# Kernel optimization log

Measured on AMD Instinct MI355X. Metric: run time of the kernel, lower is better.

The kernel has to match this reference:

```python
import jax, jax.numpy as jnp
import numpy as np

SESSION_CHANNELS = [128, 160, 192, 224, 240, 248, 252, 256]  # per-session channel counts
N_SESS = len(SESSION_CHANNELS)
B, MAX_C, MAX_T = 16, 256, 4096
HID, N_SRC = 512, 256


def setup_inputs() -> dict:
    key = jax.random.key(0)
    ks = jax.random.split(key, 7)
    session_ids = jax.random.randint(ks[0], (B,), 0, N_SESS)
    chan_table = jnp.asarray(SESSION_CHANNELS)
    channel_counts = chan_table[session_ids]
    seq_lens = jax.random.randint(ks[1], (B,), MAX_T // 2, MAX_T + 1)
    x = jax.random.normal(ks[2], (B, MAX_C, MAX_T), jnp.float32)
    # zero-pad beyond true channels and true time (as the docstring states)
    cmask = (jnp.arange(MAX_C)[None, :] < channel_counts[:, None]).astype(x.dtype)
    tmask = (jnp.arange(MAX_T)[None, :] < seq_lens[:, None]).astype(x.dtype)
    x = x * cmask[:, :, None] * tmask[:, None, :]
    # per-session Linear(num_channels -> HID), padded to MAX_C rows (torch-style uniform init)
    lim1 = 1.0 / np.sqrt(MAX_C)
    W_sess = jax.random.uniform(ks[3], (N_SESS, MAX_C, HID), jnp.float32, -lim1, lim1)
    b_sess = jax.random.uniform(ks[4], (N_SESS, HID), jnp.float32, -lim1, lim1)
    lim2 = 1.0 / np.sqrt(HID)
    W2 = jax.random.uniform(ks[5], (HID, N_SRC), jnp.float32, -lim2, lim2)
    b2 = jax.random.uniform(ks[6], (N_SRC,), jnp.float32, -lim2, lim2)
    return dict(x=x, session_ids=session_ids, channel_counts=channel_counts,
                seq_lens=seq_lens, W_sess=W_sess, b_sess=b_sess, W2=W2, b2=b2)


def reference(x, session_ids, channel_counts, seq_lens, W_sess, b_sess, W2, b2):
    # mask padded channels so the full-width contraction equals the sliced per-sample matmul
    cmask = (jnp.arange(x.shape[1])[None, :] < channel_counts[:, None]).astype(x.dtype)
    xm = x * cmask[:, :, None]                       # (B, Max_C, Max_T)
    W = W_sess[session_ids]                          # (B, Max_C, HID) gathered per sample
    b = b_sess[session_ids]                          # (B, HID)
    h = jnp.einsum('bct,bch->bht', xm, W) + b[:, :, None]
    h = jax.nn.gelu(h, approximate=False)            # torch nn.GELU default is exact erf
    out = jnp.einsum('bht,hs->bst', h, W2) + b2[None, :, None]  # (B, N_SRC, Max_T)
    tmask = (jnp.arange(x.shape[2])[None, :] < seq_lens[:, None]).astype(x.dtype)
    return out * tmask[:, None, :]
```

## Files before the change

### kernel.cpp

```cpp
#include <hip/hip_runtime.h>

typedef __attribute__((ext_vector_type(8))) _Float16 f16x8;
typedef __attribute__((ext_vector_type(4))) _Float16 f16x4;
typedef __attribute__((ext_vector_type(2))) __fp16 fp16v2;
typedef __attribute__((ext_vector_type(4))) float f32x4;

#define NB 16
#define MAXC 256
#define MAXT 4096
#define HID 512
#define NSRC 256

#define BAR() asm volatile("s_waitcnt lgkmcnt(0)\n\ts_barrier" ::: "memory")

#define MFMA(a, b, c) __builtin_amdgcn_mfma_f32_16x16x32_f16(a, b, c, 0, 0, 0)

__device__ __forceinline__ float gelu_fast(float x) {
  float p = x * x;
  float q = __builtin_fmaf(p, -0.10294336f, -2.30220778f);
  float e = __builtin_amdgcn_exp2f(x * q);
  return x * __builtin_amdgcn_rcpf(1.0f + e);
}

__global__ void transpose_cvt_kernel(const float* __restrict__ src,
                                     _Float16* __restrict__ dst, int R, int C) {
  __shared__ float tile[32][33];
  const float* s = src + (size_t)blockIdx.z * R * C;
  _Float16* d = dst + (size_t)blockIdx.z * R * C;
  int c0 = blockIdx.x * 32, r0 = blockIdx.y * 32;
  int tx = threadIdx.x, ty = threadIdx.y;
  for (int i = ty; i < 32; i += 8)
    tile[i][tx] = s[(size_t)(r0 + i) * C + (c0 + tx)];
  __syncthreads();
  for (int i = ty; i < 32; i += 8)
    d[(size_t)(c0 + i) * R + (r0 + tx)] = (_Float16)tile[tx][i];
}

__global__ __launch_bounds__(256)
void transpose_x_kernel(const float* __restrict__ x,
                        const int* __restrict__ seq_lens,
                        _Float16* __restrict__ xT) {
  int b = blockIdx.z;
  int seqlen = seq_lens[b];
  int t0 = blockIdx.x * 64;
  if (t0 >= ((seqlen + 127) & ~127)) return;
  int c0 = blockIdx.y * 64;
  __shared__ float tile[64][65];
  int tid = threadIdx.x;
  int tx = tid & 63, ty = tid >> 6;
  const float* xp = x + ((size_t)b * MAXC + c0) * MAXT + t0;
  #pragma unroll
  for (int i = 0; i < 16; ++i) {
    int c = ty + i * 4;
    tile[c][tx] = xp[(size_t)c * MAXT + tx];
  }
  __syncthreads();
  int wt = tid >> 5;
  int c2 = (tid & 31) * 2;
  _Float16* op = xT + ((size_t)b * MAXT + t0) * MAXC + c0;
  #pragma unroll
  for (int i = 0; i < 8; ++i) {
    int tl = wt + i * 8;
    fp16v2 p = __builtin_amdgcn_cvt_pkrtz(tile[c2][tl], tile[c2 + 1][tl]);
    *(fp16v2*)(op + (size_t)tl * MAXC + c2) = p;
  }
}


__global__ __launch_bounds__(256, 4)
void gemm1_kernel(const _Float16* __restrict__ xT,
                  const int* __restrict__ sess_ids,
                  const int* __restrict__ seq_lens,
                  const _Float16* __restrict__ W1t,
                  const float* __restrict__ b_sess,
                  _Float16* __restrict__ h_t) {
  int wg = blockIdx.x;
  int nt = wg & 31;
  int mt = (wg >> 5) & 3;
  int b = wg >> 7;
  int tb0 = nt * 128, h0 = mt * 128;
  int seqlen = seq_lens[b];
  if (tb0 >= seqlen) return;
  int sid = sess_ids[b];

  __shared__ _Float16 As[128 * 64];
  __shared__ _Float16 Bs[128 * 64];

  int tid = threadIdx.x;
  int lane = tid & 63, w = tid >> 6;
  int wr = w >> 1, wc = w & 1;
  int lg = lane >> 4, lr = lane & 15;

  f32x4 acc[4][4];
  #pragma unroll
  for (int mi = 0; mi < 4; ++mi) {
    f32x4 bv = *(const f32x4*)(b_sess + sid * HID + h0 + wr * 64 + mi * 16 + lg * 4);
    #pragma unroll
    for (int ni = 0; ni < 4; ++ni) acc[mi][ni] = bv;
  }

  int ar = tid >> 1, ah = tid & 1;
  const _Float16* WA = W1t + (size_t)sid * HID * MAXC + (size_t)(h0 + ar) * MAXC + ah * 32;
  const _Float16* HB = xT + ((size_t)b * MAXT + tb0 + ar) * MAXC + ah * 32;

  #pragma unroll 1
  for (int kc = 0; kc < 4; ++kc) {
    int k0 = kc * 64;
    #pragma unroll
    for (int j = 0; j < 4; ++j) {
      f16x8 v = *(const f16x8*)(WA + k0 + j * 8);
      *(f16x8*)(&As[ar * 64 + (((ah * 4 + j) ^ (ar & 7)) * 8)]) = v;
    }
    #pragma unroll
    for (int j = 0; j < 4; ++j) {
      f16x8 v = *(const f16x8*)(HB + k0 + j * 8);
      *(f16x8*)(&Bs[ar * 64 + (((ah * 4 + j) ^ (ar & 7)) * 8)]) = v;
    }
    BAR();
    #pragma unroll
    for (int slot = 0; slot < 2; ++slot) {
      f16x8 af[4], bf[4];
      #pragma unroll
      for (int mi = 0; mi < 4; ++mi) {
        int row = wr * 64 + mi * 16 + lr;
        af[mi] = *(const f16x8*)(&As[row * 64 + (((slot * 4 + lg) ^ (row & 7)) * 8)]);
      }
      #pragma unroll
      for (int ni = 0; ni < 4; ++ni) {
        int t = wc * 64 + ni * 16 + lr;
        bf[ni] = *(const f16x8*)(&Bs[t * 64 + (((slot * 4 + lg) ^ (t & 7)) * 8)]);
      }
      __builtin_amdgcn_s_setprio(1);
      #pragma unroll
      for (int mi = 0; mi < 4; ++mi)
        #pragma unroll
        for (int ni = 0; ni < 4; ++ni)
          acc[mi][ni] = MFMA(af[mi], bf[ni], acc[mi][ni]);
      __builtin_amdgcn_s_setprio(0);
    }
    BAR();
  }

  _Float16* hp = h_t + (size_t)b * MAXT * HID;
  #pragma unroll
  for (int mi = 0; mi < 4; ++mi) {
    int h = h0 + wr * 64 + mi * 16 + lg * 4;
    #pragma unroll
    for (int ni = 0; ni < 4; ++ni) {
      int t = tb0 + wc * 64 + ni * 16 + lr;
      f16x4 g;
      #pragma unroll
      for (int r = 0; r < 4; ++r) g[r] = (_Float16)gelu_fast(acc[mi][ni][r]);
      *(f16x4*)(hp + (size_t)t * HID + h) = g;
    }
  }
}

__global__ __launch_bounds__(256, 4)
void gemm2_kernel(const int* __restrict__ seq_lens,
                  const _Float16* __restrict__ W2t,
                  const float* __restrict__ b2,
                  const _Float16* __restrict__ h_t,
                  float* __restrict__ out) {
  int wg = blockIdx.x;
  int nt = wg & 31;
  int mt = (wg >> 5) & 1;
  int b = wg >> 6;
  int tb0 = nt * 128, s0 = mt * 128;
  int seqlen = seq_lens[b];
  int tid = threadIdx.x;

  if (tb0 >= seqlen) {
    int sr = tid >> 1, tq = (tid & 1) * 64;
    float* po = out + ((size_t)b * NSRC + s0 + sr) * MAXT + tb0 + tq;
    f32x4 z = {0.f, 0.f, 0.f, 0.f};
    #pragma unroll
    for (int i = 0; i < 16; ++i) *(f32x4*)(po + i * 4) = z;
    return;
  }

  __shared__ _Float16 As[128 * 64];
  __shared__ _Float16 Bs[128 * 64];

  int lane = tid & 63, w = tid >> 6;
  int wr = w >> 1, wc = w & 1;
  int lg = lane >> 4, lr = lane & 15;

  f32x4 acc[4][4];
  #pragma unroll
  for (int mi = 0; mi < 4; ++mi) {
    f32x4 bv = *(const f32x4*)(b2 + s0 + wr * 64 + mi * 16 + lg * 4);
    #pragma unroll
    for (int ni = 0; ni < 4; ++ni) acc[mi][ni] = bv;
  }

  int ar = tid >> 1, ah = tid & 1;
  const _Float16* WA = W2t + (size_t)(s0 + ar) * HID + ah * 32;
  const _Float16* HB = h_t + ((size_t)b * MAXT + tb0 + ar) * HID + ah * 32;

  #pragma unroll 1
  for (int kc = 0; kc < 8; ++kc) {
    int k0 = kc * 64;
    #pragma unroll
    for (int j = 0; j < 4; ++j) {
      f16x8 v = *(const f16x8*)(WA + k0 + j * 8);
      *(f16x8*)(&As[ar * 64 + (((ah * 4 + j) ^ (ar & 7)) * 8)]) = v;
    }
    #pragma unroll
    for (int j = 0; j < 4; ++j) {
      f16x8 v = *(const f16x8*)(HB + k0 + j * 8);
      *(f16x8*)(&Bs[ar * 64 + (((ah * 4 + j) ^ (ar & 7)) * 8)]) = v;
    }
    BAR();
    #pragma unroll
    for (int slot = 0; slot < 2; ++slot) {
      f16x8 af[4], bf[4];
      #pragma unroll
      for (int mi = 0; mi < 4; ++mi) {
        int row = wr * 64 + mi * 16 + lr;
        af[mi] = *(const f16x8*)(&As[row * 64 + (((slot * 4 + lg) ^ (row & 7)) * 8)]);
      }
      #pragma unroll
      for (int ni = 0; ni < 4; ++ni) {
        int t = wc * 64 + ni * 16 + lr;
        bf[ni] = *(const f16x8*)(&Bs[t * 64 + (((slot * 4 + lg) ^ (t & 7)) * 8)]);
      }
      __builtin_amdgcn_s_setprio(1);
      #pragma unroll
      for (int mi = 0; mi < 4; ++mi)
        #pragma unroll
        for (int ni = 0; ni < 4; ++ni)
          acc[mi][ni] = MFMA(af[mi], bf[ni], acc[mi][ni]);
      __builtin_amdgcn_s_setprio(0);
    }
    BAR();
  }

  #pragma unroll
  for (int mi = 0; mi < 4; ++mi) {
    int s = s0 + wr * 64 + mi * 16 + lg * 4;
    #pragma unroll
    for (int ni = 0; ni < 4; ++ni) {
      int t = tb0 + wc * 64 + ni * 16 + lr;
      float m = (t < seqlen) ? 1.0f : 0.0f;
      #pragma unroll
      for (int r = 0; r < 4; ++r)
        out[((size_t)b * NSRC + s + r) * MAXT + t] = acc[mi][ni][r] * m;
    }
  }
}

extern "C" void kernel_launch(void* const* d_in, const int* in_sizes, int n_in,
                              void* d_out, int out_size, void* d_ws, size_t ws_size,
                              hipStream_t stream) {
  const float* x      = (const float*)d_in[0];
  const int* sess     = (const int*)d_in[1];
  const int* seq      = (const int*)d_in[3];
  const float* W_sess = (const float*)d_in[4];
  const float* b_sess = (const float*)d_in[5];
  const float* W2     = (const float*)d_in[6];
  const float* b2     = (const float*)d_in[7];
  float* out = (float*)d_out;

  char* wp = (char*)d_ws;
  _Float16* W1t = (_Float16*)wp;                     wp += (size_t)8 * HID * MAXC * 2;
  _Float16* W2t = (_Float16*)wp;                     wp += (size_t)NSRC * HID * 2;
  _Float16* h_t = (_Float16*)wp;                     wp += (size_t)NB * MAXT * HID * 2;
  _Float16* xT  = (_Float16*)wp;

  dim3 tb(32, 8);
  transpose_cvt_kernel<<<dim3(HID / 32, MAXC / 32, 8), tb, 0, stream>>>(W_sess, W1t, MAXC, HID);
  transpose_cvt_kernel<<<dim3(NSRC / 32, HID / 32, 1), tb, 0, stream>>>(W2, W2t, HID, NSRC);
  transpose_x_kernel<<<dim3(MAXT / 64, MAXC / 64, NB), dim3(256), 0, stream>>>(x, seq, xT);

  gemm1_kernel<<<dim3(NB * 4 * 32), dim3(256), 0, stream>>>(xT, sess, seq, W1t, b_sess, h_t);
  gemm2_kernel<<<dim3(NB * 2 * 32), dim3(256), 0, stream>>>(seq, W2t, b2, h_t, out);
}
```

Measured before the change: 89.23 us.

## Register-prefetch next K tiles in both GEMMs and skip padded channel blocks in transpose

Both GEMM kernels now load the next K-chunk of A and B from global memory into registers while MFMAs run on the current shared-memory tile, then store those registers to LDS between barriers. This two-stage software pipeline is meant to hide global load latency that was previously exposed before each barrier. The x transpose kernel also reads channel_counts and writes zeros without reading x for 64-channel blocks that lie entirely beyond the sample's channel count, saving global reads. The cost is higher register pressure in the GEMMs (8 extra f16x8 vectors per thread) under launch bounds of 4 blocks.

```diff
diff --git a/kernel.cpp b/kernel.cpp
--- a/kernel.cpp
+++ b/kernel.cpp
@@ -39,14 +39,28 @@
 __global__ __launch_bounds__(256)
 void transpose_x_kernel(const float* __restrict__ x,
                         const int* __restrict__ seq_lens,
+                        const int* __restrict__ chan_counts,
                         _Float16* __restrict__ xT) {
   int b = blockIdx.z;
   int seqlen = seq_lens[b];
   int t0 = blockIdx.x * 64;
   if (t0 >= ((seqlen + 127) & ~127)) return;
   int c0 = blockIdx.y * 64;
+  int tid = threadIdx.x;
+  int wt = tid >> 5;
+  int c2 = (tid & 31) * 2;
+  _Float16* op = xT + ((size_t)b * MAXT + t0) * MAXC + c0;
+
+  if (c0 >= chan_counts[b]) {
+    #pragma unroll
+    for (int i = 0; i < 8; ++i) {
+      fp16v2 z = {(_Float16)0.f, (_Float16)0.f};
+      *(fp16v2*)(op + (size_t)(wt + i * 8) * MAXC + c2) = z;
+    }
+    return;
+  }
+
   __shared__ float tile[64][65];
-  int tid = threadIdx.x;
   int tx = tid & 63, ty = tid >> 6;
   const float* xp = x + ((size_t)b * MAXC + c0) * MAXT + t0;
   #pragma unroll
@@ -55,9 +69,6 @@
     tile[c][tx] = xp[(size_t)c * MAXT + tx];
   }
   __syncthreads();
-  int wt = tid >> 5;
-  int c2 = (tid & 31) * 2;
-  _Float16* op = xT + ((size_t)b * MAXT + t0) * MAXC + c0;
   #pragma unroll
   for (int i = 0; i < 8; ++i) {
     int tl = wt + i * 8;
@@ -103,20 +114,25 @@
   const _Float16* WA = W1t + (size_t)sid * HID * MAXC + (size_t)(h0 + ar) * MAXC + ah * 32;
   const _Float16* HB = xT + ((size_t)b * MAXT + tb0 + ar) * MAXC + ah * 32;
 
-  #pragma unroll 1
+  f16x8 RA[4], RB[4];
+  #pragma unroll
+  for (int j = 0; j < 4; ++j) RA[j] = *(const f16x8*)(WA + j * 8);
+  #pragma unroll
+  for (int j = 0; j < 4; ++j) RB[j] = *(const f16x8*)(HB + j * 8);
+  #pragma unroll
+  for (int j = 0; j < 4; ++j)
+    *(f16x8*)(&As[ar * 64 + (((ah * 4 + j) ^ (ar & 7)) * 8)]) = RA[j];
+  #pragma unroll
+  for (int j = 0; j < 4; ++j)
+    *(f16x8*)(&Bs[ar * 64 + (((ah * 4 + j) ^ (ar & 7)) * 8)]) = RB[j];
+  #pragma unroll
+  for (int j = 0; j < 4; ++j) RA[j] = *(const f16x8*)(WA + 64 + j * 8);
+  #pragma unroll
+  for (int j = 0; j < 4; ++j) RB[j] = *(const f16x8*)(HB + 64 + j * 8);
+  BAR();
+
+  #pragma unroll
   for (int kc = 0; kc < 4; ++kc) {
-    int k0 = kc * 64;
-    #pragma unroll
-    for (int j = 0; j < 4; ++j) {
-      f16x8 v = *(const f16x8*)(WA + k0 + j * 8);
-      *(f16x8*)(&As[ar * 64 + (((ah * 4 + j) ^ (ar & 7)) * 8)]) = v;
-    }
-    #pragma unroll
-    for (int j = 0; j < 4; ++j) {
-      f16x8 v = *(const f16x8*)(HB + k0 + j * 8);
-      *(f16x8*)(&Bs[ar * 64 + (((ah * 4 + j) ^ (ar & 7)) * 8)]) = v;
-    }
-    BAR();
     #pragma unroll
     for (int slot = 0; slot < 2; ++slot) {
       f16x8 af[4], bf[4];
@@ -138,7 +154,22 @@
           acc[mi][ni] = MFMA(af[mi], bf[ni], acc[mi][ni]);
       __builtin_amdgcn_s_setprio(0);
     }
-    BAR();
+    if (kc < 3) {
+      BAR();
+      #pragma unroll
+      for (int j = 0; j < 4; ++j)
+        *(f16x8*)(&As[ar * 64 + (((ah * 4 + j) ^ (ar & 7)) * 8)]) = RA[j];
+      #pragma unroll
+      for (int j = 0; j < 4; ++j)
+        *(f16x8*)(&Bs[ar * 64 + (((ah * 4 + j) ^ (ar & 7)) * 8)]) = RB[j];
+      if (kc < 2) {
+        #pragma unroll
+        for (int j = 0; j < 4; ++j) RA[j] = *(const f16x8*)(WA + (kc + 2) * 64 + j * 8);
+        #pragma unroll
+        for (int j = 0; j < 4; ++j) RB[j] = *(const f16x8*)(HB + (kc + 2) * 64 + j * 8);
+      }
+      BAR();
+    }
   }
 
   _Float16* hp = h_t + (size_t)b * MAXT * HID;
@@ -198,20 +229,25 @@
   const _Float16* WA = W2t + (size_t)(s0 + ar) * HID + ah * 32;
   const _Float16* HB = h_t + ((size_t)b * MAXT + tb0 + ar) * HID + ah * 32;
 
-  #pragma unroll 1
+  f16x8 RA[4], RB[4];
+  #pragma unroll
+  for (int j = 0; j < 4; ++j) RA[j] = *(const f16x8*)(WA + j * 8);
+  #pragma unroll
+  for (int j = 0; j < 4; ++j) RB[j] = *(const f16x8*)(HB + j * 8);
+  #pragma unroll
+  for (int j = 0; j < 4; ++j)
+    *(f16x8*)(&As[ar * 64 + (((ah * 4 + j) ^ (ar & 7)) * 8)]) = RA[j];
+  #pragma unroll
+  for (int j = 0; j < 4; ++j)
+    *(f16x8*)(&Bs[ar * 64 + (((ah * 4 + j) ^ (ar & 7)) * 8)]) = RB[j];
+  #pragma unroll
+  for (int j = 0; j < 4; ++j) RA[j] = *(const f16x8*)(WA + 64 + j * 8);
+  #pragma unroll
+  for (int j = 0; j < 4; ++j) RB[j] = *(const f16x8*)(HB + 64 + j * 8);
+  BAR();
+
+  #pragma unroll
   for (int kc = 0; kc < 8; ++kc) {
-    int k0 = kc * 64;
-    #pragma unroll
-    for (int j = 0; j < 4; ++j) {
-      f16x8 v = *(const f16x8*)(WA + k0 + j * 8);
-      *(f16x8*)(&As[ar * 64 + (((ah * 4 + j) ^ (ar & 7)) * 8)]) = v;
-    }
-    #pragma unroll
-    for (int j = 0; j < 4; ++j) {
-      f16x8 v = *(const f16x8*)(HB + k0 + j * 8);
-      *(f16x8*)(&Bs[ar * 64 + (((ah * 4 + j) ^ (ar & 7)) * 8)]) = v;
-    }
-    BAR();
     #pragma unroll
     for (int slot = 0; slot < 2; ++slot) {
       f16x8 af[4], bf[4];
@@ -233,7 +269,22 @@
           acc[mi][ni] = MFMA(af[mi], bf[ni], acc[mi][ni]);
       __builtin_amdgcn_s_setprio(0);
     }
-    BAR();
+    if (kc < 7) {
+      BAR();
+      #pragma unroll
+      for (int j = 0; j < 4; ++j)
+        *(f16x8*)(&As[ar * 64 + (((ah * 4 + j) ^ (ar & 7)) * 8)]) = RA[j];
+      #pragma unroll
+      for (int j = 0; j < 4; ++j)
+        *(f16x8*)(&Bs[ar * 64 + (((ah * 4 + j) ^ (ar & 7)) * 8)]) = RB[j];
+      if (kc < 6) {
+        #pragma unroll
+        for (int j = 0; j < 4; ++j) RA[j] = *(const f16x8*)(WA + (kc + 2) * 64 + j * 8);
+        #pragma unroll
+        for (int j = 0; j < 4; ++j) RB[j] = *(const f16x8*)(HB + (kc + 2) * 64 + j * 8);
+      }
+      BAR();
+    }
   }
 
   #pragma unroll
@@ -255,6 +306,7 @@
                               hipStream_t stream) {
   const float* x      = (const float*)d_in[0];
   const int* sess     = (const int*)d_in[1];
+  const int* ccnt     = (const int*)d_in[2];
   const int* seq      = (const int*)d_in[3];
   const float* W_sess = (const float*)d_in[4];
   const float* b_sess = (const float*)d_in[5];
@@ -271,7 +323,7 @@
   dim3 tb(32, 8);
   transpose_cvt_kernel<<<dim3(HID / 32, MAXC / 32, 8), tb, 0, stream>>>(W_sess, W1t, MAXC, HID);
   transpose_cvt_kernel<<<dim3(NSRC / 32, HID / 32, 1), tb, 0, stream>>>(W2, W2t, HID, NSRC);
-  transpose_x_kernel<<<dim3(MAXT / 64, MAXC / 64, NB), dim3(256), 0, stream>>>(x, seq, xT);
+  transpose_x_kernel<<<dim3(MAXT / 64, MAXC / 64, NB), dim3(256), 0, stream>>>(x, seq, ccnt, xT);
 
   gemm1_kernel<<<dim3(NB * 4 * 32), dim3(256), 0, stream>>>(xT, sess, seq, W1t, b_sess, h_t);
   gemm2_kernel<<<dim3(NB * 2 * 32), dim3(256), 0, stream>>>(seq, W2t, b2, h_t, out);
```

Result: slower. 276.2 us (+209.5%).

## Load GEMM tiles via direct global-to-LDS loads and skip padded channel blocks

Applied to the files above, without the earlier changes.

Both GEMM kernels now stage A/B tiles with global_load_lds (direct DMA into LDS) instead of loading into registers and storing to LDS, with the XOR swizzle applied on the global side. The transpose kernel writes zeros for 64-channel blocks beyond the sample's channel count and skips reading x there. This is meant to cut VGPR pressure and LDS store instructions, and to avoid reading padded input. It is still single-buffered, though, with a full vmcnt wait before compute, so loads do not overlap MFMA work.

```diff
diff --git a/kernel.cpp b/kernel.cpp
--- a/kernel.cpp
+++ b/kernel.cpp
@@ -11,9 +11,15 @@
 #define HID 512
 #define NSRC 256
 
+#define BARV() asm volatile("s_waitcnt vmcnt(0) lgkmcnt(0)\n\ts_barrier" ::: "memory")
 #define BAR() asm volatile("s_waitcnt lgkmcnt(0)\n\ts_barrier" ::: "memory")
 
 #define MFMA(a, b, c) __builtin_amdgcn_mfma_f32_16x16x32_f16(a, b, c, 0, 0, 0)
+
+typedef __attribute__((address_space(1))) const void gconst_void;
+typedef __attribute__((address_space(3))) void lds_void;
+#define GLOAD16(gp, lp) \
+  __builtin_amdgcn_global_load_lds((gconst_void*)(gp), (lds_void*)(lp), 16, 0, 0)
 
 __device__ __forceinline__ float gelu_fast(float x) {
   float p = x * x;
@@ -39,14 +45,28 @@
 __global__ __launch_bounds__(256)
 void transpose_x_kernel(const float* __restrict__ x,
                         const int* __restrict__ seq_lens,
+                        const int* __restrict__ chan_counts,
                         _Float16* __restrict__ xT) {
   int b = blockIdx.z;
   int seqlen = seq_lens[b];
   int t0 = blockIdx.x * 64;
   if (t0 >= ((seqlen + 127) & ~127)) return;
   int c0 = blockIdx.y * 64;
+  int tid = threadIdx.x;
+  int wt = tid >> 5;
+  int c2 = (tid & 31) * 2;
+  _Float16* op = xT + ((size_t)b * MAXT + t0) * MAXC + c0;
+
+  if (c0 >= chan_counts[b]) {
+    #pragma unroll
+    for (int i = 0; i < 8; ++i) {
+      fp16v2 z = {(_Float16)0.f, (_Float16)0.f};
+      *(fp16v2*)(op + (size_t)(wt + i * 8) * MAXC + c2) = z;
+    }
+    return;
+  }
+
   __shared__ float tile[64][65];
-  int tid = threadIdx.x;
   int tx = tid & 63, ty = tid >> 6;
   const float* xp = x + ((size_t)b * MAXC + c0) * MAXT + t0;
   #pragma unroll
@@ -55,9 +75,6 @@
     tile[c][tx] = xp[(size_t)c * MAXT + tx];
   }
   __syncthreads();
-  int wt = tid >> 5;
-  int c2 = (tid & 31) * 2;
-  _Float16* op = xT + ((size_t)b * MAXT + t0) * MAXC + c0;
   #pragma unroll
   for (int i = 0; i < 8; ++i) {
     int tl = wt + i * 8;
@@ -99,24 +116,27 @@
     for (int ni = 0; ni < 4; ++ni) acc[mi][ni] = bv;
   }
 
-  int ar = tid >> 1, ah = tid & 1;
-  const _Float16* WA = W1t + (size_t)sid * HID * MAXC + (size_t)(h0 + ar) * MAXC + ah * 32;
-  const _Float16* HB = xT + ((size_t)b * MAXT + tb0 + ar) * MAXC + ah * 32;
+  int rsub = lane >> 3;
+  int swb = ((lane & 7) ^ rsub) * 16;
+  const char* gA = (const char*)(W1t + (size_t)sid * HID * MAXC + (size_t)h0 * MAXC)
+                   + (size_t)(w * 32 + rsub) * 512 + swb;
+  const char* gB = (const char*)(xT + ((size_t)b * MAXT + tb0) * MAXC)
+                   + (size_t)(w * 32 + rsub) * 512 + swb;
+  char* lA = (char*)As + w * 4096;
+  char* lB = (char*)Bs + w * 4096;
+
+#define STAGE1(kc)                                                   \
+  _Pragma("unroll")                                                  \
+  for (int j = 0; j < 4; ++j) {                                      \
+    GLOAD16(gA + (size_t)(kc)*128 + (size_t)j * 8 * 512, lA + j * 1024); \
+    GLOAD16(gB + (size_t)(kc)*128 + (size_t)j * 8 * 512, lB + j * 1024); \
+  }
+
+  STAGE1(0);
+  BARV();
 
   #pragma unroll 1
   for (int kc = 0; kc < 4; ++kc) {
-    int k0 = kc * 64;
-    #pragma unroll
-    for (int j = 0; j < 4; ++j) {
-      f16x8 v = *(const f16x8*)(WA + k0 + j * 8);
-      *(f16x8*)(&As[ar * 64 + (((ah * 4 + j) ^ (ar & 7)) * 8)]) = v;
-    }
-    #pragma unroll
-    for (int j = 0; j < 4; ++j) {
-      f16x8 v = *(const f16x8*)(HB + k0 + j * 8);
-      *(f16x8*)(&Bs[ar * 64 + (((ah * 4 + j) ^ (ar & 7)) * 8)]) = v;
-    }
-    BAR();
     #pragma unroll
     for (int slot = 0; slot < 2; ++slot) {
       f16x8 af[4], bf[4];
@@ -138,7 +158,11 @@
           acc[mi][ni] = MFMA(af[mi], bf[ni], acc[mi][ni]);
       __builtin_amdgcn_s_setprio(0);
     }
-    BAR();
+    if (kc < 3) {
+      BAR();
+      STAGE1(kc + 1);
+      BARV();
+    }
   }
 
   _Float16* hp = h_t + (size_t)b * MAXT * HID;
@@ -194,24 +218,27 @@
     for (int ni = 0; ni < 4; ++ni) acc[mi][ni] = bv;
   }
 
-  int ar = tid >> 1, ah = tid & 1;
-  const _Float16* WA = W2t + (size_t)(s0 + ar) * HID + ah * 32;
-  const _Float16* HB = h_t + ((size_t)b * MAXT + tb0 + ar) * HID + ah * 32;
+  int rsub = lane >> 3;
+  int swb = ((lane & 7) ^ rsub) * 16;
+  const char* gA = (const char*)(W2t + (size_t)s0 * HID)
+                   + (size_t)(w * 32 + rsub) * 1024 + swb;
+  const char* gB = (const char*)(h_t + ((size_t)b * MAXT + tb0) * HID)
+                   + (size_t)(w * 32 + rsub) * 1024 + swb;
+  char* lA = (char*)As + w * 4096;
+  char* lB = (char*)Bs + w * 4096;
+
+#define STAGE2(kc)                                                    \
+  _Pragma("unroll")                                                   \
+  for (int j = 0; j < 4; ++j) {                                       \
+    GLOAD16(gA + (size_t)(kc)*128 + (size_t)j * 8 * 1024, lA + j * 1024); \
+    GLOAD16(gB + (size_t)(kc)*128 + (size_t)j * 8 * 1024, lB + j * 1024); \
+  }
+
+  STAGE2(0);
+  BARV();
 
   #pragma unroll 1
   for (int kc = 0; kc < 8; ++kc) {
-    int k0 = kc * 64;
-    #pragma unroll
-    for (int j = 0; j < 4; ++j) {
-      f16x8 v = *(const f16x8*)(WA + k0 + j * 8);
-      *(f16x8*)(&As[ar * 64 + (((ah * 4 + j) ^ (ar & 7)) * 8)]) = v;
-    }
-    #pragma unroll
-    for (int j = 0; j < 4; ++j) {
-      f16x8 v = *(const f16x8*)(HB + k0 + j * 8);
-      *(f16x8*)(&Bs[ar * 64 + (((ah * 4 + j) ^ (ar & 7)) * 8)]) = v;
-    }
-    BAR();
     #pragma unroll
     for (int slot = 0; slot < 2; ++slot) {
       f16x8 af[4], bf[4];
@@ -233,7 +260,11 @@
           acc[mi][ni] = MFMA(af[mi], bf[ni], acc[mi][ni]);
       __builtin_amdgcn_s_setprio(0);
     }
-    BAR();
+    if (kc < 7) {
+      BAR();
+      STAGE2(kc + 1);
+      BARV();
+    }
   }
 
   #pragma unroll
@@ -255,6 +286,7 @@
                               hipStream_t stream) {
   const float* x      = (const float*)d_in[0];
   const int* sess     = (const int*)d_in[1];
+  const int* ccnt     = (const int*)d_in[2];
   const int* seq      = (const int*)d_in[3];
   const float* W_sess = (const float*)d_in[4];
   const float* b_sess = (const float*)d_in[5];
@@ -271,7 +303,7 @@
   dim3 tb(32, 8);
   transpose_cvt_kernel<<<dim3(HID / 32, MAXC / 32, 8), tb, 0, stream>>>(W_sess, W1t, MAXC, HID);
   transpose_cvt_kernel<<<dim3(NSRC / 32, HID / 32, 1), tb, 0, stream>>>(W2, W2t, HID, NSRC);
-  transpose_x_kernel<<<dim3(MAXT / 64, MAXC / 64, NB), dim3(256), 0, stream>>>(x, seq, xT);
+  transpose_x_kernel<<<dim3(MAXT / 64, MAXC / 64, NB), dim3(256), 0, stream>>>(x, seq, ccnt, xT);
 
   gemm1_kernel<<<dim3(NB * 4 * 32), dim3(256), 0, stream>>>(xT, sess, seq, W1t, b_sess, h_t);
   gemm2_kernel<<<dim3(NB * 2 * 32), dim3(256), 0, stream>>>(seq, W2t, b2, h_t, out);
```

Result: faster. 82.13 us (-7.9%).
